# Kernel tuning notes

Hardware: AMD Instinct MI355X
Metric: run time of the kernel (lower is better)

The kernel has to match this reference:

```python
import jax, jax.numpy as jnp
import numpy as np

NUM_TREES = 64
INPUT_DIM = 512
DEPTH = 6
NUM_CLASSES = 10
INIT_TEMP = 2.0
SHRINKAGE = 0.3
BN_EPS = 1e-5
ATTN_HIDDEN = 128


def setup_inputs() -> dict:
    key = jax.random.key(0)
    ks = jax.random.split(key, 10)
    B = 16384
    num_nodes = 2 ** DEPTH - 1   # 63
    num_leaves = 2 ** DEPTH      # 64
    x = jax.random.normal(ks[0], (B, INPUT_DIM), dtype=jnp.float32)
    # Attention network params (Linear stored as [in, out])
    attn_w1 = jax.random.normal(ks[1], (INPUT_DIM, ATTN_HIDDEN), dtype=jnp.float32) / np.sqrt(INPUT_DIM)
    attn_b1 = jnp.zeros((ATTN_HIDDEN,), jnp.float32)
    bn_gamma = jnp.ones((ATTN_HIDDEN,), jnp.float32)
    bn_beta = jnp.zeros((ATTN_HIDDEN,), jnp.float32)
    bn_mean = jnp.zeros((ATTN_HIDDEN,), jnp.float32)   # eval-mode running stats
    bn_var = jnp.ones((ATTN_HIDDEN,), jnp.float32)
    attn_w2 = jax.random.normal(ks[2], (ATTN_HIDDEN, NUM_TREES), dtype=jnp.float32) / np.sqrt(ATTN_HIDDEN)
    attn_b2 = jnp.zeros((NUM_TREES,), jnp.float32)
    # Stacked per-tree params
    tree_w = jax.random.normal(ks[3], (NUM_TREES, num_nodes, INPUT_DIM), dtype=jnp.float32)
    tree_b = jnp.zeros((NUM_TREES, num_nodes), jnp.float32)
    tree_temp = jnp.full((NUM_TREES,), INIT_TEMP, jnp.float32)
    leaf_values = jax.random.normal(ks[4], (NUM_TREES, num_leaves, NUM_CLASSES), dtype=jnp.float32)
    residual_weights = jax.nn.sigmoid(jax.random.normal(ks[5], (NUM_TREES,), dtype=jnp.float32))
    return {
        'x': x, 'attn_w1': attn_w1, 'attn_b1': attn_b1,
        'bn_gamma': bn_gamma, 'bn_beta': bn_beta, 'bn_mean': bn_mean, 'bn_var': bn_var,
        'attn_w2': attn_w2, 'attn_b2': attn_b2,
        'tree_w': tree_w, 'tree_b': tree_b, 'tree_temp': tree_temp,
        'leaf_values': leaf_values, 'residual_weights': residual_weights,
    }


def _forward(x, attn_w1, attn_b1, bn_gamma, bn_beta, bn_mean, bn_var,
             attn_w2, attn_b2, tree_w, tree_b, tree_temp, leaf_values, residual_weights):
    # --- attention weights over trees ---
    h = jax.nn.relu(x @ attn_w1 + attn_b1)
    h = (h - bn_mean) * jax.lax.rsqrt(bn_var + BN_EPS) * bn_gamma + bn_beta  # BatchNorm1d eval
    attn = jax.nn.softmax(h @ attn_w2 + attn_b2, axis=1)  # [B, T]

    # --- soft-tree ensemble (eval mode: no dropout, no tree skipping) ---
    missing = jnp.isnan(x)
    xc = jnp.where(missing, 0.0, x)
    missing_any = jnp.any(missing, axis=1)  # [B]

    # All split logits in one GEMM: [B, T, num_nodes]
    logits = jnp.einsum('bd,tnd->btn', xc, tree_w) + tree_b[None]
    dec = jax.nn.sigmoid(logits / tree_temp[None, :, None])
    dec = jnp.where(missing_any[:, None, None], 0.5, dec)

    B, T = x.shape[0], tree_w.shape[0]
    routing = jnp.ones((B, T, 1), x.dtype)
    for lvl in range(DEPTH):
        d = dec[:, :, 2 ** lvl - 1: 2 ** (lvl + 1) - 1]  # [B, T, 2^lvl]
        # matches torch: routing.repeat(1,2) * cat([d, 1-d])
        routing = jnp.concatenate([routing, routing], -1) * jnp.concatenate([d, 1.0 - d], -1)
    # routing now [B, T, 2^DEPTH] = leaf probabilities

    tree_out = jnp.einsum('btl,tlc->btc', routing, leaf_values)  # [B, T, C]
    coef = SHRINKAGE * residual_weights  # [T]
    pred = jnp.einsum('bt,t,btc->bc', attn, coef, tree_out)
    return jax.nn.softmax(pred, axis=1)  # multiclass_classification


def reference(x, attn_w1, attn_b1, bn_gamma, bn_beta, bn_mean, bn_var,
              attn_w2, attn_b2, tree_w, tree_b, tree_temp, leaf_values, residual_weights):
    return _forward(x, attn_w1, attn_b1, bn_gamma, bn_beta, bn_mean, bn_var,
                    attn_w2, attn_b2, tree_w, tree_b, tree_temp, leaf_values, residual_weights)
```

## Files before the change

kernel.cpp:

```cpp
#include <hip/hip_runtime.h>
#include <hip/hip_fp16.h>
#include <stdint.h>

#define IN_DIM 512
#define NT 64
#define AH 128
#define NCLS 10
#define BN_EPS_C 1e-5f
#define SHRINK 0.3f
#define HSTRIDE 66
#define HPLANE 8448

typedef __bf16 bf16x8 __attribute__((ext_vector_type(8)));
typedef float f32x4 __attribute__((ext_vector_type(4)));
typedef unsigned int u32x4 __attribute__((ext_vector_type(4)));

__device__ __forceinline__ unsigned short f2bf(float f) {
  unsigned u = __builtin_bit_cast(unsigned, f);
  u += 0x7fffu + ((u >> 16) & 1u);
  return (unsigned short)(u >> 16);
}

__device__ __forceinline__ float bflo(unsigned w) {
  return __builtin_bit_cast(float, w << 16);
}
__device__ __forceinline__ float bfhi(unsigned w) {
  return __builtin_bit_cast(float, w & 0xffff0000u);
}

__device__ __forceinline__ void gload_lds16(const void* g, void* l) {
  __builtin_amdgcn_global_load_lds(
      (const __attribute__((address_space(1))) void*)g,
      (__attribute__((address_space(3))) void*)l, 16, 0, 0);
}

__device__ __forceinline__ bf16x8 frag_ld(const char* lds, int r, int q) {
  return *reinterpret_cast<const bf16x8*>(lds + r * 128 + ((q ^ (r & 7)) * 16));
}

__device__ __forceinline__ void stage_trees(const unsigned short* Ak,
                                            const unsigned short* Bk,
                                            char* As, char* Bs,
                                            int wid, int sub, int cpos) {
#pragma unroll
  for (int i = 0; i < 4; i++) {
    int seg = wid * 4 + i;
    int r = seg * 8 + sub;
    int cg = cpos ^ (r & 7);
    gload_lds16(Ak + r * 512 + cg * 8, As + seg * 1024);
    gload_lds16(Bk + r * 512 + cg * 8, Bs + seg * 1024);
  }
}

__global__ void __launch_bounds__(256) k_prep(
    const float* __restrict__ tw, unsigned short* __restrict__ twb,
    const float* __restrict__ w1, unsigned short* __restrict__ w1t) {
  int b = blockIdx.x;
  if (b < 1024) {
    int tid = b * 256 + threadIdx.x;
    int o = tid * 8;
    int k = o & 511;
    int nt = o >> 9;
    int node = nt & 63, t = nt >> 6;
    union { unsigned short s[8]; u32x4 u; } pk;
    if (node < 63) {
      const float* p = tw + ((t * 63 + node) * 512 + k);
      float4 a = *(const float4*)p, bb = *(const float4*)(p + 4);
      float v[8] = {a.x, a.y, a.z, a.w, bb.x, bb.y, bb.z, bb.w};
#pragma unroll
      for (int i = 0; i < 8; i++) pk.s[i] = f2bf(v[i]);
    } else {
#pragma unroll
      for (int i = 0; i < 8; i++) pk.s[i] = 0;
    }
    *reinterpret_cast<u32x4*>(twb + o) = pk.u;
  } else {
    int tid = (b - 1024) * 256 + threadIdx.x;
    int k = tid & 511, n = tid >> 9;
    w1t[n * 512 + k] = f2bf(w1[k * 128 + n]);
  }
}

__global__ void __launch_bounds__(256) k_attn(
    const float* __restrict__ x, unsigned short* __restrict__ xc,
    float* __restrict__ flags,
    const unsigned short* __restrict__ w1t,
    const float* __restrict__ b1, const float* __restrict__ gam,
    const float* __restrict__ bet, const float* __restrict__ mu,
    const float* __restrict__ var, const float* __restrict__ w2,
    const float* __restrict__ b2, const float* __restrict__ rw,
    float* __restrict__ wbt) {
  __shared__ __align__(16) char smem[59392];
  char* As = smem;
  char* Bs = smem + 8192;
  unsigned short* hb  = (unsigned short*)(smem + 24576);
  unsigned short* w2s = (unsigned short*)(smem + 41984);
  int lane = threadIdx.x & 63, wid = threadIdx.x >> 6;
  int bm0 = blockIdx.x * 64;
  int m = lane & 15, q = lane >> 4;
  int sub = lane >> 3, cpos = lane & 7;

  for (int i = 0; i < 16; ++i) {
    int r = bm0 + wid * 16 + i;
    const float* px = x + (size_t)r * 512 + lane * 8;
    float4 a = *(const float4*)px;
    float4 bb = *(const float4*)(px + 4);
    float v[8] = {a.x, a.y, a.z, a.w, bb.x, bb.y, bb.z, bb.w};
    bool nan_any = false;
    union { unsigned short s[8]; u32x4 u; } pk;
#pragma unroll
    for (int j = 0; j < 8; j++) {
      bool n = (v[j] != v[j]);
      nan_any |= n;
      pk.s[j] = f2bf(n ? 0.f : v[j]);
    }
    *reinterpret_cast<u32x4*>(xc + (size_t)r * 512 + lane * 8) = pk.u;
    unsigned long long bal = __ballot(nan_any);
    if (lane == 0) flags[r] = bal ? 1.f : 0.f;
  }

  for (int i = threadIdx.x; i < AH * NT; i += 256) {
    int k = i >> 6, n = i & 63;
    w2s[n * 136 + k] = f2bf(w2[i]);
  }
  __syncthreads();

  f32x4 acc[8];
#pragma unroll
  for (int j = 0; j < 8; j++) acc[j] = f32x4{0.f, 0.f, 0.f, 0.f};
  const unsigned short* Ag = xc + (size_t)bm0 * 512;

  for (int ko = 0; ko < 8; ++ko) {
    const unsigned short* Ak = Ag + ko * 64;
    const unsigned short* Bk = w1t + ko * 64;
#pragma unroll
    for (int i = 0; i < 2; i++) {
      int seg = wid * 2 + i;
      int r = seg * 8 + sub;
      int cg = cpos ^ (r & 7);
      gload_lds16(Ak + r * 512 + cg * 8, As + seg * 1024);
    }
#pragma unroll
    for (int i = 0; i < 4; i++) {
      int seg = wid * 4 + i;
      int r = seg * 8 + sub;
      int cg = cpos ^ (r & 7);
      gload_lds16(Bk + r * 512 + cg * 8, Bs + seg * 1024);
    }
    __syncthreads();
#pragma unroll
    for (int ks = 0; ks < 2; ++ks) {
      bf16x8 af = frag_ld(As, wid * 16 + m, ks * 4 + q);
#pragma unroll
      for (int ni = 0; ni < 8; ni++) {
        bf16x8 bfr = frag_ld(Bs, ni * 16 + m, ks * 4 + q);
        acc[ni] = __builtin_amdgcn_mfma_f32_16x16x32_bf16(af, bfr, acc[ni], 0, 0, 0);
      }
    }
    __syncthreads();
  }

#pragma unroll
  for (int ni = 0; ni < 8; ni++) {
    int col = ni * 16 + m;
    float bb = b1[col], ga = gam[col], be = bet[col], mm = mu[col];
    float iv = rsqrtf(var[col] + BN_EPS_C);
#pragma unroll
    for (int r4 = 0; r4 < 4; r4++) {
      int rl = wid * 16 + q * 4 + r4;
      float v = acc[ni][r4] + bb;
      v = fmaxf(v, 0.f);
      v = (v - mm) * iv * ga + be;
      hb[rl * 136 + col] = f2bf(v);
    }
  }

  f32x4 acc2[4];
#pragma unroll
  for (int nt = 0; nt < 4; nt++) acc2[nt] = f32x4{0.f, 0.f, 0.f, 0.f};
#pragma unroll
  for (int ks = 0; ks < 4; ++ks) {
    bf16x8 af = *reinterpret_cast<const bf16x8*>(hb + (wid * 16 + m) * 136 + ks * 32 + q * 8);
#pragma unroll
    for (int nt = 0; nt < 4; nt++) {
      bf16x8 bfr = *reinterpret_cast<const bf16x8*>(w2s + (nt * 16 + m) * 136 + ks * 32 + q * 8);
      acc2[nt] = __builtin_amdgcn_mfma_f32_16x16x32_bf16(af, bfr, acc2[nt], 0, 0, 0);
    }
  }

  float b2v[4], cfv[4];
#pragma unroll
  for (int nt = 0; nt < 4; nt++) {
    int col = nt * 16 + m;
    b2v[nt] = b2[col];
    cfv[nt] = SHRINK * rw[col];
  }
#pragma unroll
  for (int reg = 0; reg < 4; ++reg) {
    float s0 = acc2[0][reg] + b2v[0];
    float s1 = acc2[1][reg] + b2v[1];
    float s2 = acc2[2][reg] + b2v[2];
    float s3 = acc2[3][reg] + b2v[3];
    float mx = fmaxf(fmaxf(s0, s1), fmaxf(s2, s3));
#pragma unroll
    for (int o = 1; o < 16; o <<= 1) mx = fmaxf(mx, __shfl_xor(mx, o));
    float e0 = __expf(s0 - mx), e1 = __expf(s1 - mx);
    float e2 = __expf(s2 - mx), e3 = __expf(s3 - mx);
    float sm = e0 + e1 + e2 + e3;
#pragma unroll
    for (int o = 1; o < 16; o <<= 1) sm += __shfl_xor(sm, o);
    float inv = 1.f / sm;
    int row = bm0 + wid * 16 + q * 4 + reg;
    wbt[row * NT + m]      = e0 * inv * cfv[0];
    wbt[row * NT + 16 + m] = e1 * inv * cfv[1];
    wbt[row * NT + 32 + m] = e2 * inv * cfv[2];
    wbt[row * NT + 48 + m] = e3 * inv * cfv[3];
  }
}

__global__ void __launch_bounds__(256) k_trees(
    const unsigned short* __restrict__ xc,
    const unsigned short* __restrict__ twb,
    const float* __restrict__ tree_b,
    const float* __restrict__ tree_temp,
    const float* __restrict__ leaf,
    const float* __restrict__ wbt,
    const float* __restrict__ flags,
    unsigned short* __restrict__ part) {
  __shared__ __align__(16) char smem[65536];
  char* A0 = smem;
  char* B0 = smem + 16384;
  char* A1 = smem + 32768;
  char* B1 = smem + 49152;
  unsigned short* dh = (unsigned short*)smem;
  int lane = threadIdx.x & 63, wid = threadIdx.x >> 6;
  int bm0 = blockIdx.y * 128;
  int t0 = blockIdx.x * 2;
  int m = lane & 15, q = lane >> 4;
  int sub = lane >> 3, cpos = lane & 7;
  int wr = wid >> 1, wc = wid & 1;
  int row_l = threadIdx.x & 127;
  int h = __builtin_amdgcn_readfirstlane((int)(threadIdx.x >> 7));
  int grow = bm0 + row_l;

  f32x4 acc[4][4];
#pragma unroll
  for (int i = 0; i < 4; i++)
#pragma unroll
    for (int j = 0; j < 4; j++) acc[i][j] = f32x4{0.f, 0.f, 0.f, 0.f};

  const unsigned short* Ag = xc + (size_t)bm0 * 512;
  const unsigned short* Bg = twb + (size_t)t0 * 64 * 512;

  stage_trees(Ag, Bg, A0, B0, wid, sub, cpos);
  __syncthreads();

#pragma unroll
  for (int ko = 0; ko < 8; ++ko) {
    char* As = (ko & 1) ? A1 : A0;
    char* Bs = (ko & 1) ? B1 : B0;
    if (ko < 7) {
      char* An = (ko & 1) ? A0 : A1;
      char* Bn = (ko & 1) ? B0 : B1;
      stage_trees(Ag + (ko + 1) * 64, Bg + (ko + 1) * 64, An, Bn, wid, sub, cpos);
    }
#pragma unroll
    for (int ks = 0; ks < 2; ++ks) {
      bf16x8 af[4], bfr[4];
#pragma unroll
      for (int mi = 0; mi < 4; mi++) af[mi] = frag_ld(As, wr * 64 + mi * 16 + m, ks * 4 + q);
#pragma unroll
      for (int ni = 0; ni < 4; ni++) bfr[ni] = frag_ld(Bs, wc * 64 + ni * 16 + m, ks * 4 + q);
#pragma unroll
      for (int mi = 0; mi < 4; mi++)
#pragma unroll
        for (int ni = 0; ni < 4; ni++)
          acc[mi][ni] = __builtin_amdgcn_mfma_f32_16x16x32_bf16(af[mi], bfr[ni], acc[mi][ni], 0, 0, 0);
    }
    __syncthreads();
  }

  float flv[4][4];
#pragma unroll
  for (int mi = 0; mi < 4; mi++) {
    float4 f0 = *(const float4*)(flags + bm0 + wr * 64 + mi * 16 + q * 4);
    flv[mi][0] = f0.x; flv[mi][1] = f0.y; flv[mi][2] = f0.z; flv[mi][3] = f0.w;
  }
  float2 wpair = *(const float2*)(wbt + grow * 64 + t0);

  {
    int t = t0 + wc;
    float nk2 = -1.44269504089f / tree_temp[t];
    float ncb[4];
#pragma unroll
    for (int ni = 0; ni < 4; ni++) {
      int node = ni * 16 + m;
      ncb[ni] = ((node < 63) ? tree_b[t * 63 + node] : 0.f) * nk2;
    }
#pragma unroll
    for (int mi = 0; mi < 4; mi++) {
#pragma unroll
      for (int ni = 0; ni < 4; ni++) {
        int node = ni * 16 + m;
        f32x4 a = acc[mi][ni];
#pragma unroll
        for (int r4 = 0; r4 < 4; r4++) {
          int row = wr * 64 + mi * 16 + q * 4 + r4;
          float e = exp2f(fmaf(a[r4], nk2, ncb[ni]));
          float sig = __builtin_amdgcn_rcpf(1.f + e);
          unsigned short hv = __half_as_ushort(__float2half(sig));
          hv = (flv[mi][r4] != 0.f) ? (unsigned short)0x3800 : hv;
          dh[wc * HPLANE + row * HSTRIDE + node + 1] = hv;
        }
      }
    }
  }
  __syncthreads();

  float pc[10];
#pragma unroll
  for (int c = 0; c < 10; c++) pc[c] = 0.f;

#pragma unroll
  for (int tt = 0; tt < 2; ++tt) {
    int t = t0 + tt;
    const unsigned short* dr = dh + tt * HPLANE + row_l * HSTRIDE;
    float R[16];
    {
      float d0 = __half2float(__ushort_as_half(dr[1]));
      R[0] = d0;
      R[1] = 1.f - d0;
    }
#pragma unroll
    for (int L = 1; L <= 3; ++L) {
      int half = 1 << L;
#pragma unroll
      for (int g = 0; g < half; g += 2) {
        float2 dd = __half22float2(*reinterpret_cast<const __half2*>(dr + half + g));
        float ra = R[g] * dd.x;
        R[g + half] = R[g] - ra;
        R[g] = ra;
        float rb = R[g + 1] * dd.y;
        R[g + 1 + half] = R[g + 1] - rb;
        R[g + 1] = rb;
      }
    }
#pragma unroll
    for (int p = 0; p < 16; p += 2) {
      float2 dd = __half22float2(*reinterpret_cast<const __half2*>(dr + 16 + p));
      float da = h ? (1.f - dd.x) : dd.x;
      float db = h ? (1.f - dd.y) : dd.y;
      R[p] *= da;
      R[p + 1] *= db;
    }
    float a10[10];
#pragma unroll
    for (int c = 0; c < 10; c++) a10[c] = 0.f;
    const float* Lf = leaf + (size_t)(t * 64 + 16 * h) * 10;
#pragma unroll
    for (int p = 0; p < 16; p += 2) {
      float2 dd = __half22float2(*reinterpret_cast<const __half2*>(dr + 32 + 16 * h + p));
      float rla = R[p] * dd.x, rra = R[p] - rla;
      float rlb = R[p + 1] * dd.y, rrb = R[p + 1] - rlb;
#pragma unroll
      for (int c = 0; c < 10; c++) {
        float s = fmaf(rla, Lf[p * 10 + c], a10[c]);
        s = fmaf(rra, Lf[320 + p * 10 + c], s);
        s = fmaf(rlb, Lf[p * 10 + 10 + c], s);
        a10[c] = fmaf(rrb, Lf[330 + p * 10 + c], s);
      }
    }
    float w = tt ? wpair.y : wpair.x;
#pragma unroll
    for (int c = 0; c < 10; c++) pc[c] = fmaf(w, a10[c], pc[c]);
  }

  __syncthreads();
  float* redbuf = reinterpret_cast<float*>(smem);
  if (h == 1) {
#pragma unroll
    for (int c = 0; c < 10; c++) redbuf[row_l * 10 + c] = pc[c];
  }
  __syncthreads();
  if (h == 0) {
    unsigned short* po = part + ((size_t)grow * 32 + blockIdx.x) * 10;
    unsigned wdw[5];
#pragma unroll
    for (int k = 0; k < 5; k++) {
      unsigned lo = f2bf(pc[2 * k] + redbuf[row_l * 10 + 2 * k]);
      unsigned hi = f2bf(pc[2 * k + 1] + redbuf[row_l * 10 + 2 * k + 1]);
      wdw[k] = lo | (hi << 16);
    }
    unsigned* pu = reinterpret_cast<unsigned*>(po);
#pragma unroll
    for (int k = 0; k < 5; k++) pu[k] = wdw[k];
  }
}

__global__ void __launch_bounds__(128) k_finish(const unsigned short* __restrict__ part,
                                               float* __restrict__ out) {
  int row = blockIdx.x * 128 + threadIdx.x;
  const uint4* pu = reinterpret_cast<const uint4*>(part + (size_t)row * 320);
  float v[10];
#pragma unroll
  for (int c = 0; c < 10; c++) v[c] = 0.f;
#pragma unroll
  for (int ch = 0; ch < 8; ++ch) {
    uint4 w0 = pu[ch * 5 + 0];
    uint4 w1 = pu[ch * 5 + 1];
    uint4 w2 = pu[ch * 5 + 2];
    uint4 w3 = pu[ch * 5 + 3];
    uint4 w4 = pu[ch * 5 + 4];
    unsigned dw[20] = {w0.x, w0.y, w0.z, w0.w, w1.x, w1.y, w1.z, w1.w,
                       w2.x, w2.y, w2.z, w2.w, w3.x, w3.y, w3.z, w3.w,
                       w4.x, w4.y, w4.z, w4.w};
#pragma unroll
    for (int d = 0; d < 20; d++) {
      int k = d % 5;
      v[2 * k] += bflo(dw[d]);
      v[2 * k + 1] += bfhi(dw[d]);
    }
  }
  float mx = -1e30f;
#pragma unroll
  for (int c = 0; c < 10; c++) mx = fmaxf(mx, v[c]);
  float sm = 0.f;
#pragma unroll
  for (int c = 0; c < 10; c++) {
    v[c] = __expf(v[c] - mx);
    sm += v[c];
  }
  float inv = 1.f / sm;
#pragma unroll
  for (int c = 0; c < 10; c++) out[row * 10 + c] = v[c] * inv;
}

extern "C" void kernel_launch(void* const* d_in, const int* in_sizes, int n_in,
                              void* d_out, int out_size, void* d_ws, size_t ws_size,
                              hipStream_t stream) {
  const float* x    = (const float*)d_in[0];
  const float* w1   = (const float*)d_in[1];
  const float* b1   = (const float*)d_in[2];
  const float* gam  = (const float*)d_in[3];
  const float* bet  = (const float*)d_in[4];
  const float* mu   = (const float*)d_in[5];
  const float* var  = (const float*)d_in[6];
  const float* w2   = (const float*)d_in[7];
  const float* b2   = (const float*)d_in[8];
  const float* tw   = (const float*)d_in[9];
  const float* tb   = (const float*)d_in[10];
  const float* temp = (const float*)d_in[11];
  const float* leaf = (const float*)d_in[12];
  const float* rw   = (const float*)d_in[13];
  float* out = (float*)d_out;

  char* ws = (char*)d_ws;
  unsigned short* xc  = (unsigned short*)(ws);
  unsigned short* twb = (unsigned short*)(ws + 16777216);
  unsigned short* w1t = (unsigned short*)(ws + 20971520);
  float* wbt  = (float*)(ws + 21102592);
  float* flg  = (float*)(ws + 25296896);
  unsigned short* part = (unsigned short*)(ws + 25362432);

  k_prep<<<1280, 256, 0, stream>>>(tw, twb, w1, w1t);
  k_attn<<<256, 256, 0, stream>>>(x, xc, flg, w1t, b1, gam, bet, mu, var,
                                  w2, b2, rw, wbt);
  dim3 g2(32, 128);
  k_trees<<<g2, 256, 0, stream>>>(xc, twb, tb, temp, leaf, wbt, flg, part);
  k_finish<<<128, 128, 0, stream>>>(part, out);
}
```

Before: 254.4 us.

## Stage A tiles through registers to cut LDS to 48KB

Replaces the double-buffered LDS staging of the x tile with a register prefetch into a single LDS A buffer, while B stays double-buffered via direct global-to-LDS loads. This shrinks shared memory per block from 64KB to 48KB, likely to let more blocks reside per CU. In exchange it adds an extra barrier per k-step, extra VGPR pressure for the prefetched fragments, and LDS write instructions issued from registers.

```diff
diff --git a/kernel.cpp b/kernel.cpp
--- a/kernel.cpp
+++ b/kernel.cpp
@@ -36,20 +36,6 @@
 
 __device__ __forceinline__ bf16x8 frag_ld(const char* lds, int r, int q) {
   return *reinterpret_cast<const bf16x8*>(lds + r * 128 + ((q ^ (r & 7)) * 16));
-}
-
-__device__ __forceinline__ void stage_trees(const unsigned short* Ak,
-                                            const unsigned short* Bk,
-                                            char* As, char* Bs,
-                                            int wid, int sub, int cpos) {
-#pragma unroll
-  for (int i = 0; i < 4; i++) {
-    int seg = wid * 4 + i;
-    int r = seg * 8 + sub;
-    int cg = cpos ^ (r & 7);
-    gload_lds16(Ak + r * 512 + cg * 8, As + seg * 1024);
-    gload_lds16(Bk + r * 512 + cg * 8, Bs + seg * 1024);
-  }
 }
 
 __global__ void __launch_bounds__(256) k_prep(
@@ -227,11 +213,10 @@
     const float* __restrict__ wbt,
     const float* __restrict__ flags,
     unsigned short* __restrict__ part) {
-  __shared__ __align__(16) char smem[65536];
-  char* A0 = smem;
+  __shared__ __align__(16) char smem[49152];
+  char* As = smem;
   char* B0 = smem + 16384;
-  char* A1 = smem + 32768;
-  char* B1 = smem + 49152;
+  char* B1 = smem + 32768;
   unsigned short* dh = (unsigned short*)smem;
   int lane = threadIdx.x & 63, wid = threadIdx.x >> 6;
   int bm0 = blockIdx.y * 128;
@@ -252,17 +237,38 @@
   const unsigned short* Ag = xc + (size_t)bm0 * 512;
   const unsigned short* Bg = twb + (size_t)t0 * 64 * 512;
 
-  stage_trees(Ag, Bg, A0, B0, wid, sub, cpos);
+  bf16x8 areg[4];
+
+#pragma unroll
+  for (int i = 0; i < 4; i++) {
+    int seg = wid * 4 + i;
+    int r = seg * 8 + sub;
+    int cg = cpos ^ (r & 7);
+    areg[i] = *reinterpret_cast<const bf16x8*>(Ag + r * 512 + cg * 8);
+    gload_lds16(Bg + r * 512 + cg * 8, B0 + seg * 1024);
+  }
+#pragma unroll
+  for (int i = 0; i < 4; i++) {
+    int seg = wid * 4 + i;
+    *reinterpret_cast<bf16x8*>(As + seg * 1024 + lane * 16) = areg[i];
+  }
   __syncthreads();
 
 #pragma unroll
   for (int ko = 0; ko < 8; ++ko) {
-    char* As = (ko & 1) ? A1 : A0;
     char* Bs = (ko & 1) ? B1 : B0;
     if (ko < 7) {
-      char* An = (ko & 1) ? A0 : A1;
       char* Bn = (ko & 1) ? B0 : B1;
-      stage_trees(Ag + (ko + 1) * 64, Bg + (ko + 1) * 64, An, Bn, wid, sub, cpos);
+      const unsigned short* An = Ag + (ko + 1) * 64;
+      const unsigned short* Bk = Bg + (ko + 1) * 64;
+#pragma unroll
+      for (int i = 0; i < 4; i++) {
+        int seg = wid * 4 + i;
+        int r = seg * 8 + sub;
+        int cg = cpos ^ (r & 7);
+        areg[i] = *reinterpret_cast<const bf16x8*>(An + r * 512 + cg * 8);
+        gload_lds16(Bk + r * 512 + cg * 8, Bn + seg * 1024);
+      }
     }
 #pragma unroll
     for (int ks = 0; ks < 2; ++ks) {
@@ -278,6 +284,14 @@
           acc[mi][ni] = __builtin_amdgcn_mfma_f32_16x16x32_bf16(af[mi], bfr[ni], acc[mi][ni], 0, 0, 0);
     }
     __syncthreads();
+    if (ko < 7) {
+#pragma unroll
+      for (int i = 0; i < 4; i++) {
+        int seg = wid * 4 + i;
+        *reinterpret_cast<bf16x8*>(As + seg * 1024 + lane * 16) = areg[i];
+      }
+      __syncthreads();
+    }
   }
 
   float flv[4][4];
```

Measured after the change: 249.5 us. About the same (-1.9%).

## Fuse tree-weight prep into attention kernel and convert W1 on the fly

Applied to the files above, without the earlier changes.

Merges the prep and attention kernels into one launch. Blocks at index 256 and above convert the tree weights to bf16, and the first 256 blocks run the attention MLP. The W1 transpose buffer is gone: each attention block reads W1 in fp32 straight from global memory, converts it to bf16 in registers, and writes it into LDS, prefetching the next K-slice while the current one is in use. This removes one launch and one intermediate buffer. In exchange, every attention block re-reads W1 with strided, uncoalesced accesses, and the large shared-memory allocation now also applies to the prep blocks, which limits their occupancy.

```diff
diff --git a/kernel.cpp b/kernel.cpp
--- a/kernel.cpp
+++ b/kernel.cpp
@@ -52,12 +52,20 @@
   }
 }
 
-__global__ void __launch_bounds__(256) k_prep(
-    const float* __restrict__ tw, unsigned short* __restrict__ twb,
-    const float* __restrict__ w1, unsigned short* __restrict__ w1t) {
-  int b = blockIdx.x;
-  if (b < 1024) {
-    int tid = b * 256 + threadIdx.x;
+__global__ void __launch_bounds__(256) k_attn_prep(
+    const float* __restrict__ x, unsigned short* __restrict__ xc,
+    float* __restrict__ flags,
+    const float* __restrict__ w1,
+    const float* __restrict__ b1, const float* __restrict__ gam,
+    const float* __restrict__ bet, const float* __restrict__ mu,
+    const float* __restrict__ var, const float* __restrict__ w2,
+    const float* __restrict__ b2, const float* __restrict__ rw,
+    float* __restrict__ wbt,
+    const float* __restrict__ tw, unsigned short* __restrict__ twb) {
+  __shared__ __align__(16) char smem[59392];
+
+  if (blockIdx.x >= 256) {
+    int tid = (blockIdx.x - 256) * 256 + threadIdx.x;
     int o = tid * 8;
     int k = o & 511;
     int nt = o >> 9;
@@ -74,23 +82,9 @@
       for (int i = 0; i < 8; i++) pk.s[i] = 0;
     }
     *reinterpret_cast<u32x4*>(twb + o) = pk.u;
-  } else {
-    int tid = (b - 1024) * 256 + threadIdx.x;
-    int k = tid & 511, n = tid >> 9;
-    w1t[n * 512 + k] = f2bf(w1[k * 128 + n]);
-  }
-}
-
-__global__ void __launch_bounds__(256) k_attn(
-    const float* __restrict__ x, unsigned short* __restrict__ xc,
-    float* __restrict__ flags,
-    const unsigned short* __restrict__ w1t,
-    const float* __restrict__ b1, const float* __restrict__ gam,
-    const float* __restrict__ bet, const float* __restrict__ mu,
-    const float* __restrict__ var, const float* __restrict__ w2,
-    const float* __restrict__ b2, const float* __restrict__ rw,
-    float* __restrict__ wbt) {
-  __shared__ __align__(16) char smem[59392];
+    return;
+  }
+
   char* As = smem;
   char* Bs = smem + 8192;
   unsigned short* hb  = (unsigned short*)(smem + 24576);
@@ -130,9 +124,20 @@
   for (int j = 0; j < 8; j++) acc[j] = f32x4{0.f, 0.f, 0.f, 0.f};
   const unsigned short* Ag = xc + (size_t)bm0 * 512;
 
+  int cgB = cpos ^ sub;
+  float wv[4][8];
+
+#pragma unroll
+  for (int i = 0; i < 4; i++) {
+    int r = (wid * 4 + i) * 8 + sub;
+    const float* p = w1 + (size_t)(cgB * 8) * 128 + r;
+#pragma unroll
+    for (int j = 0; j < 8; j++) wv[i][j] = p[j * 128];
+  }
+
   for (int ko = 0; ko < 8; ++ko) {
+    if (ko > 0) __syncthreads();
     const unsigned short* Ak = Ag + ko * 64;
-    const unsigned short* Bk = w1t + ko * 64;
 #pragma unroll
     for (int i = 0; i < 2; i++) {
       int seg = wid * 2 + i;
@@ -143,9 +148,19 @@
 #pragma unroll
     for (int i = 0; i < 4; i++) {
       int seg = wid * 4 + i;
-      int r = seg * 8 + sub;
-      int cg = cpos ^ (r & 7);
-      gload_lds16(Bk + r * 512 + cg * 8, Bs + seg * 1024);
+      union { unsigned short s[8]; u32x4 u; } pk;
+#pragma unroll
+      for (int j = 0; j < 8; j++) pk.s[j] = f2bf(wv[i][j]);
+      *reinterpret_cast<u32x4*>(Bs + seg * 1024 + lane * 16) = pk.u;
+    }
+    if (ko < 7) {
+#pragma unroll
+      for (int i = 0; i < 4; i++) {
+        int r = (wid * 4 + i) * 8 + sub;
+        const float* p = w1 + (size_t)((ko + 1) * 64 + cgB * 8) * 128 + r;
+#pragma unroll
+        for (int j = 0; j < 8; j++) wv[i][j] = p[j * 128];
+      }
     }
     __syncthreads();
 #pragma unroll
@@ -157,7 +172,6 @@
         acc[ni] = __builtin_amdgcn_mfma_f32_16x16x32_bf16(af, bfr, acc[ni], 0, 0, 0);
       }
     }
-    __syncthreads();
   }
 
 #pragma unroll
@@ -457,14 +471,12 @@
   char* ws = (char*)d_ws;
   unsigned short* xc  = (unsigned short*)(ws);
   unsigned short* twb = (unsigned short*)(ws + 16777216);
-  unsigned short* w1t = (unsigned short*)(ws + 20971520);
   float* wbt  = (float*)(ws + 21102592);
   float* flg  = (float*)(ws + 25296896);
   unsigned short* part = (unsigned short*)(ws + 25362432);
 
-  k_prep<<<1280, 256, 0, stream>>>(tw, twb, w1, w1t);
-  k_attn<<<256, 256, 0, stream>>>(x, xc, flg, w1t, b1, gam, bet, mu, var,
-                                  w2, b2, rw, wbt);
+  k_attn_prep<<<1280, 256, 0, stream>>>(x, xc, flg, w1, b1, gam, bet, mu, var,
+                                        w2, b2, rw, wbt, tw, twb);
   dim3 g2(32, 128);
   k_trees<<<g2, 256, 0, stream>>>(xc, twb, tb, temp, leaf, wbt, flg, part);
   k_finish<<<128, 128, 0, stream>>>(part, out);
```

Result: slower. 263.8 us (+3.7%).
